# Kernel tuning notes

Measured on AMD Instinct MI355X. Metric: run time of the kernel, lower is better.

Reference implementation:

```python
import jax, jax.numpy as jnp
import numpy as np

B, H, S, D = 1, 16, 2048, 128
NUM_DOCS = 4


def setup_inputs() -> dict:
    key = jax.random.key(0)
    kq, kk, kv = jax.random.split(key, 3)
    q = jax.random.normal(kq, (B, H, S, D), dtype=jnp.float32)
    k = jax.random.normal(kk, (B, H, S, D), dtype=jnp.float32)
    v = jax.random.normal(kv, (B, H, S, D), dtype=jnp.float32)
    # Document boundaries within the packed sequence (as produced by _get_offsets):
    # starts at 0, ends at total token count. 4 equal docs of length 512.
    offsets = jnp.array([0, 512, 1024, 1536, 2048], dtype=jnp.int64)
    return {"q": q, "k": k, "v": v, "offsets": offsets}


def reference(q, k, v, offsets):
    # Block-causal SDPA: token i attends to token j iff j <= i and both are
    # in the same document (documents delimited by `offsets`). This matches
    # nested-tensor SDPA with is_causal=True over the jagged documents.
    _, _, S_, D_ = q.shape
    pos = jnp.arange(S_)
    seg = jnp.searchsorted(offsets, pos, side="right")  # [S] document id per token
    mask = (seg[:, None] == seg[None, :]) & (pos[None, :] <= pos[:, None])  # [S,S]
    scale = 1.0 / jnp.sqrt(jnp.asarray(D_, q.dtype))
    scores = jnp.einsum("bhsd,bhtd->bhst", q, k) * scale  # [B,H,S,S]
    scores = jnp.where(mask[None, None], scores, jnp.finfo(q.dtype).min)
    attn = jax.nn.softmax(scores, axis=-1)
    return jnp.einsum("bhst,bhtd->bhsd", attn, v)
```

## Files before the change

kernel.cpp:

```cpp
#include <hip/hip_runtime.h>
#include <hip/hip_bf16.h>
#include <math.h>

#define NH 16
#define SL 2048
#define DM 128
#define KVB 64

typedef float f32x4 __attribute__((ext_vector_type(4)));
typedef short s16x8 __attribute__((ext_vector_type(8)));
typedef short s16x4 __attribute__((ext_vector_type(4)));

static __device__ __forceinline__ short f2bf(float f) {
  __hip_bfloat16 h = __float2bfloat16(f);
  return __builtin_bit_cast(short, h);
}

__global__ __launch_bounds__(256) void attn_mfma(
    const float* __restrict__ qg,
    const float* __restrict__ kg,
    const float* __restrict__ vg,
    const int* __restrict__ offs, int n_off,
    float* __restrict__ out)
{
  __shared__ __align__(16) char Kb[64 * 128 * 2];
  __shared__ __align__(16) char Vb[128 * 64 * 2];
  __shared__ __align__(16) char Pb[4][16 * 64 * 2];

  const int t    = threadIdx.x;
  const int lane = t & 63;
  const int w    = t >> 6;
  const int col  = lane & 15;
  const int g    = lane >> 4;

  const int h  = blockIdx.x & 15;
  const int qb = 31 - (blockIdx.x >> 4);
  const int q0 = qb * 64;

  const float* qh = qg + (size_t)h * SL * DM;
  const float* kh = kg + (size_t)h * SL * DM;
  const float* vh = vg + (size_t)h * SL * DM;

  const float scale = 0.08838834764831843f;

  const int qrow = q0 + 16 * w + col;
  int qstart = 0;
  for (int i = 0; i < n_off; ++i) { int o = offs[i]; if (o <= qrow) qstart = o; }
  int kv_lo = 0;
  for (int i = 0; i < n_off; ++i) { int o = offs[i]; if (o <= q0) kv_lo = o; }

  s16x8 qf[4];
  #pragma unroll
  for (int kk = 0; kk < 4; ++kk) {
    const float* qp = qh + (size_t)qrow * DM + 32 * kk + 8 * g;
    f32x4 lo = *(const f32x4*)qp;
    f32x4 hi = *(const f32x4*)(qp + 4);
    s16x8 f;
    f[0] = f2bf(lo[0] * scale); f[1] = f2bf(lo[1] * scale);
    f[2] = f2bf(lo[2] * scale); f[3] = f2bf(lo[3] * scale);
    f[4] = f2bf(hi[0] * scale); f[5] = f2bf(hi[1] * scale);
    f[6] = f2bf(hi[2] * scale); f[7] = f2bf(hi[3] * scale);
    qf[kk] = f;
  }

  f32x4 acc[8];
  #pragma unroll
  for (int dt = 0; dt < 8; ++dt) { f32x4 z = {0.f, 0.f, 0.f, 0.f}; acc[dt] = z; }
  float m_ = -1e30f, l_ = 0.f;

  char* pb = &Pb[w][0];

  for (int kv0 = kv_lo; kv0 < q0 + 64; kv0 += KVB) {
    {
      const float* ks = kh + (size_t)kv0 * DM;
      const float* vs = vh + (size_t)kv0 * DM;
      const int d0 = (t & 31) * 4;
      const int r0 = t >> 5;
      #pragma unroll
      for (int ri = 0; ri < 8; ++ri) {
        int r = r0 + 8 * ri;
        f32x4 f = *(const f32x4*)(ks + (size_t)r * DM + d0);
        s16x4 b;
        b[0] = f2bf(f[0]); b[1] = f2bf(f[1]); b[2] = f2bf(f[2]); b[3] = f2bf(f[3]);
        *(s16x4*)(Kb + ((r * 256 + d0 * 2) ^ ((r & 7) << 4))) = b;
      }
      const int rot = (t >> 1) & 3;
      #pragma unroll
      for (int ki = 0; ki < 2; ++ki) {
        int k0 = r0 * 4 + 32 * ki;
        f32x4 a0 = *(const f32x4*)(vs + (size_t)(k0 + 0) * DM + d0);
        f32x4 a1 = *(const f32x4*)(vs + (size_t)(k0 + 1) * DM + d0);
        f32x4 a2 = *(const f32x4*)(vs + (size_t)(k0 + 2) * DM + d0);
        f32x4 a3 = *(const f32x4*)(vs + (size_t)(k0 + 3) * DM + d0);
        #pragma unroll
        for (int di = 0; di < 4; ++di) {
          int dd = (di + rot) & 3;
          int d = d0 + dd;
          s16x4 b;
          b[0] = f2bf(a0[dd]); b[1] = f2bf(a1[dd]); b[2] = f2bf(a2[dd]); b[3] = f2bf(a3[dd]);
          *(s16x4*)(Vb + ((d * 128 + k0 * 2) ^ ((d & 7) << 4))) = b;
        }
      }
    }
    __syncthreads();

    f32x4 st[4];
    #pragma unroll
    for (int kt = 0; kt < 4; ++kt) { f32x4 z = {0.f, 0.f, 0.f, 0.f}; st[kt] = z; }
    __builtin_amdgcn_s_setprio(1);
    #pragma unroll
    for (int kt = 0; kt < 4; ++kt) {
      int row = kt * 16 + col;
      #pragma unroll
      for (int kk = 0; kk < 4; ++kk) {
        s16x8 kf = *(const s16x8*)(Kb + ((row * 256 + 64 * kk + 16 * g) ^ ((row & 7) << 4)));
        st[kt] = __builtin_amdgcn_mfma_f32_16x16x32_bf16(kf, qf[kk], st[kt], 0, 0, 0);
      }
    }
    __builtin_amdgcn_s_setprio(0);

    float cm = -3.0e38f;
    #pragma unroll
    for (int kt = 0; kt < 4; ++kt) {
      #pragma unroll
      for (int r = 0; r < 4; ++r) {
        int kpos = kv0 + kt * 16 + 4 * g + r;
        float x = st[kt][r];
        bool ok = (kpos <= qrow) && (kpos >= qstart);
        x = ok ? x : -3.0e38f;
        st[kt][r] = x;
        cm = fmaxf(cm, x);
      }
    }
    cm = fmaxf(cm, __shfl_xor(cm, 16));
    cm = fmaxf(cm, __shfl_xor(cm, 32));
    float mn = fmaxf(m_, cm);
    float al = __expf(m_ - mn);
    m_ = mn;
    float psum = 0.f;
    #pragma unroll
    for (int kt = 0; kt < 4; ++kt) {
      s16x4 pk;
      #pragma unroll
      for (int r = 0; r < 4; ++r) {
        float p = __expf(st[kt][r] - mn);
        psum += p;
        pk[r] = f2bf(p);
      }
      *(s16x4*)(pb + ((col * 128 + 32 * kt + 8 * g) ^ ((col & 7) << 4))) = pk;
    }
    psum += __shfl_xor(psum, 16);
    psum += __shfl_xor(psum, 32);
    l_ = l_ * al + psum;

    #pragma unroll
    for (int r = 0; r < 4; ++r) {
      float ar = __shfl(al, 4 * g + r);
      #pragma unroll
      for (int dt = 0; dt < 8; ++dt) acc[dt][r] *= ar;
    }

    asm volatile("s_waitcnt lgkmcnt(0)" ::: "memory");
    __builtin_amdgcn_sched_barrier(0);

    __builtin_amdgcn_s_setprio(1);
    #pragma unroll
    for (int ksel = 0; ksel < 2; ++ksel) {
      s16x8 pa = *(const s16x8*)(pb + ((col * 128 + 64 * ksel + 16 * g) ^ ((col & 7) << 4)));
      #pragma unroll
      for (int dt = 0; dt < 8; ++dt) {
        int d = dt * 16 + col;
        s16x8 vf = *(const s16x8*)(Vb + ((d * 128 + 64 * ksel + 16 * g) ^ ((d & 7) << 4)));
        acc[dt] = __builtin_amdgcn_mfma_f32_16x16x32_bf16(pa, vf, acc[dt], 0, 0, 0);
      }
    }
    __builtin_amdgcn_s_setprio(0);
    __syncthreads();
  }

  #pragma unroll
  for (int r = 0; r < 4; ++r) {
    float lr  = __shfl(l_, 4 * g + r);
    float inv = 1.f / lr;
    int row   = q0 + 16 * w + 4 * g + r;
    float* op = out + ((size_t)h * SL + row) * DM + col;
    #pragma unroll
    for (int dt = 0; dt < 8; ++dt) op[dt * 16] = acc[dt][r] * inv;
  }
}

extern "C" void kernel_launch(void* const* d_in, const int* in_sizes, int n_in,
                              void* d_out, int out_size, void* d_ws, size_t ws_size,
                              hipStream_t stream) {
  const float* q = (const float*)d_in[0];
  const float* k = (const float*)d_in[1];
  const float* v = (const float*)d_in[2];
  const int* offs = (const int*)d_in[3];
  const int n_off = in_sizes[3];
  float* out = (float*)d_out;

  const int blocks = NH * (SL / 64);
  attn_mfma<<<blocks, 256, 0, stream>>>(q, k, v, offs, n_off, out);
}
```

Baseline: 31.34 us.

## Pre-convert K/V to swizzled bf16 and double-buffer tiles via global_load_lds

Adds a separate pre-pass kernel that converts K and V to bf16 once, into the pre-swizzled shared-memory layout in workspace. The attention kernel then streams these tiles straight into double-buffered LDS with global_load_lds, prefetching the next tile while it computes the current one. This removes the repeated per-block fp32 load and convert work and overlaps loads with compute. The price is an extra kernel launch, an extra round trip of K/V through global memory, and doubled LDS use that may lower occupancy. It also remaps the block index so work is interleaved within each document, and keeps a fallback kernel for when the workspace is too small.

```diff
diff --git a/kernel.cpp b/kernel.cpp
--- a/kernel.cpp
+++ b/kernel.cpp
@@ -5,7 +5,6 @@
 #define NH 16
 #define SL 2048
 #define DM 128
-#define KVB 64
 
 typedef float f32x4 __attribute__((ext_vector_type(4)));
 typedef short s16x8 __attribute__((ext_vector_type(8)));
@@ -16,7 +15,227 @@
   return __builtin_bit_cast(short, h);
 }
 
-__global__ __launch_bounds__(256) void attn_mfma(
+__global__ __launch_bounds__(256) void convert_kv(
+    const float* __restrict__ kg, const float* __restrict__ vg,
+    char* __restrict__ kbf, char* __restrict__ vbf)
+{
+  const int t = threadIdx.x;
+  const int h = blockIdx.x & 15;
+  const int T = blockIdx.x >> 4;
+  const float* ks = kg + ((size_t)h * SL + (size_t)T * 64) * DM;
+  const float* vs = vg + ((size_t)h * SL + (size_t)T * 64) * DM;
+  char* kc = kbf + (((size_t)h * 32 + T) << 14);
+  char* vc = vbf + (((size_t)h * 32 + T) << 14);
+  const int d0 = (t & 31) * 4;
+  const int r0 = t >> 5;
+  #pragma unroll
+  for (int ri = 0; ri < 8; ++ri) {
+    int r = r0 + 8 * ri;
+    f32x4 f = *(const f32x4*)(ks + (size_t)r * DM + d0);
+    s16x4 b;
+    b[0] = f2bf(f[0]); b[1] = f2bf(f[1]); b[2] = f2bf(f[2]); b[3] = f2bf(f[3]);
+    *(s16x4*)(kc + ((r * 256 + d0 * 2) ^ ((r & 7) << 4))) = b;
+  }
+  #pragma unroll
+  for (int ki = 0; ki < 2; ++ki) {
+    int k0 = r0 * 4 + 32 * ki;
+    f32x4 a0 = *(const f32x4*)(vs + (size_t)(k0 + 0) * DM + d0);
+    f32x4 a1 = *(const f32x4*)(vs + (size_t)(k0 + 1) * DM + d0);
+    f32x4 a2 = *(const f32x4*)(vs + (size_t)(k0 + 2) * DM + d0);
+    f32x4 a3 = *(const f32x4*)(vs + (size_t)(k0 + 3) * DM + d0);
+    #pragma unroll
+    for (int dd = 0; dd < 4; ++dd) {
+      int d = d0 + dd;
+      s16x4 b;
+      b[0] = f2bf(a0[dd]); b[1] = f2bf(a1[dd]); b[2] = f2bf(a2[dd]); b[3] = f2bf(a3[dd]);
+      *(s16x4*)(vc + ((d * 128 + k0 * 2) ^ ((d & 7) << 4))) = b;
+    }
+  }
+}
+
+#define GLDS16(gsrc, lbase) \
+  __builtin_amdgcn_global_load_lds( \
+      (const __attribute__((address_space(1))) void*)(gsrc), \
+      (__attribute__((address_space(3))) void*)(lbase), 16, 0, 0)
+
+__global__ __launch_bounds__(256) void attn_mfma2(
+    const float* __restrict__ qg,
+    const char* __restrict__ kbf, const char* __restrict__ vbf,
+    const int* __restrict__ offs, int n_off,
+    float* __restrict__ out)
+{
+  __shared__ __align__(16) char Kb[2][16384];
+  __shared__ __align__(16) char Vb[2][16384];
+  __shared__ __align__(16) char Pb[4][2048];
+
+  const int t    = threadIdx.x;
+  const int lane = t & 63;
+  const int w    = t >> 6;
+  const int col  = lane & 15;
+  const int g    = lane >> 4;
+
+  const int blk = blockIdx.x;
+  const int z = blk >> 8;
+  const int y = (blk >> 4) & 15;
+  const int h = blk & 15;
+  const int dno = y >> 2, u = y & 3;
+  const int p = z ? u : 7 - u;
+  const int q0 = (dno * 8 + p) * 64;
+
+  const float* qh = qg + (size_t)h * SL * DM;
+  const float scale = 0.08838834764831843f;
+
+  const int qrow = q0 + 16 * w + col;
+  int qstart = 0;
+  for (int i = 0; i < n_off; ++i) { int o = offs[i]; if (o <= qrow) qstart = o; }
+  int kv_lo = 0;
+  for (int i = 0; i < n_off; ++i) { int o = offs[i]; if (o <= q0) kv_lo = o; }
+  const int ntiles = ((q0 + 64) - kv_lo) >> 6;
+  const int T0 = kv_lo >> 6;
+
+  const char* kc = kbf + (((size_t)h * 32) << 14);
+  const char* vc = vbf + (((size_t)h * 32) << 14);
+
+#define STAGE(T, B) do {                                                     \
+    const char* _ks = kc + (((size_t)(T)) << 14);                            \
+    const char* _vs = vc + (((size_t)(T)) << 14);                            \
+    _Pragma("unroll")                                                        \
+    for (int _i = 0; _i < 4; ++_i) {                                         \
+      const int _lo = (w + 4 * _i) << 10;                                    \
+      GLDS16(_ks + _lo + lane * 16, &Kb[B][_lo]);                            \
+      GLDS16(_vs + _lo + lane * 16, &Vb[B][_lo]);                            \
+    }                                                                        \
+  } while (0)
+
+  f32x4 qlo[4], qhi[4];
+  #pragma unroll
+  for (int kk = 0; kk < 4; ++kk) {
+    const float* qp = qh + (size_t)qrow * DM + 32 * kk + 8 * g;
+    qlo[kk] = *(const f32x4*)qp;
+    qhi[kk] = *(const f32x4*)(qp + 4);
+  }
+
+  STAGE(T0, 0);
+
+  s16x8 qf[4];
+  #pragma unroll
+  for (int kk = 0; kk < 4; ++kk) {
+    s16x8 f;
+    f[0] = f2bf(qlo[kk][0] * scale); f[1] = f2bf(qlo[kk][1] * scale);
+    f[2] = f2bf(qlo[kk][2] * scale); f[3] = f2bf(qlo[kk][3] * scale);
+    f[4] = f2bf(qhi[kk][0] * scale); f[5] = f2bf(qhi[kk][1] * scale);
+    f[6] = f2bf(qhi[kk][2] * scale); f[7] = f2bf(qhi[kk][3] * scale);
+    qf[kk] = f;
+  }
+
+  f32x4 acc[8];
+  #pragma unroll
+  for (int dt = 0; dt < 8; ++dt) { f32x4 zv = {0.f, 0.f, 0.f, 0.f}; acc[dt] = zv; }
+  float m_ = -1e30f, l_ = 0.f;
+
+  char* pb = &Pb[w][0];
+  int buf = 0;
+
+  for (int it = 0; it < ntiles; ++it) {
+    const int kv0 = kv_lo + (it << 6);
+    if (it + 1 < ntiles) {
+      STAGE(T0 + it + 1, buf ^ 1);
+      asm volatile("s_waitcnt vmcnt(8)" ::: "memory");
+    } else {
+      asm volatile("s_waitcnt vmcnt(0)" ::: "memory");
+    }
+    __builtin_amdgcn_sched_barrier(0);
+    __builtin_amdgcn_s_barrier();
+
+    f32x4 st[4];
+    #pragma unroll
+    for (int kt = 0; kt < 4; ++kt) { f32x4 zv = {0.f, 0.f, 0.f, 0.f}; st[kt] = zv; }
+    __builtin_amdgcn_s_setprio(1);
+    #pragma unroll
+    for (int kt = 0; kt < 4; ++kt) {
+      int row = kt * 16 + col;
+      #pragma unroll
+      for (int kk = 0; kk < 4; ++kk) {
+        s16x8 kf = *(const s16x8*)(&Kb[buf][0] + ((row * 256 + 64 * kk + 16 * g) ^ ((row & 7) << 4)));
+        st[kt] = __builtin_amdgcn_mfma_f32_16x16x32_bf16(kf, qf[kk], st[kt], 0, 0, 0);
+      }
+    }
+    __builtin_amdgcn_s_setprio(0);
+
+    float cm = -3.0e38f;
+    #pragma unroll
+    for (int kt = 0; kt < 4; ++kt) {
+      #pragma unroll
+      for (int r = 0; r < 4; ++r) {
+        int kpos = kv0 + kt * 16 + 4 * g + r;
+        float x = st[kt][r];
+        bool ok = (kpos <= qrow) && (kpos >= qstart);
+        x = ok ? x : -3.0e38f;
+        st[kt][r] = x;
+        cm = fmaxf(cm, x);
+      }
+    }
+    cm = fmaxf(cm, __shfl_xor(cm, 16));
+    cm = fmaxf(cm, __shfl_xor(cm, 32));
+    float mn = fmaxf(m_, cm);
+    float al = __expf(m_ - mn);
+    m_ = mn;
+    float psum = 0.f;
+    #pragma unroll
+    for (int kt = 0; kt < 4; ++kt) {
+      s16x4 pk;
+      #pragma unroll
+      for (int r = 0; r < 4; ++r) {
+        float pe = __expf(st[kt][r] - mn);
+        psum += pe;
+        pk[r] = f2bf(pe);
+      }
+      *(s16x4*)(pb + ((col * 128 + 32 * kt + 8 * g) ^ ((col & 7) << 4))) = pk;
+    }
+    psum += __shfl_xor(psum, 16);
+    psum += __shfl_xor(psum, 32);
+    l_ = l_ * al + psum;
+
+    #pragma unroll
+    for (int r = 0; r < 4; ++r) {
+      float ar = __shfl(al, 4 * g + r);
+      #pragma unroll
+      for (int dt = 0; dt < 8; ++dt) acc[dt][r] *= ar;
+    }
+
+    asm volatile("s_waitcnt lgkmcnt(0)" ::: "memory");
+    __builtin_amdgcn_sched_barrier(0);
+
+    __builtin_amdgcn_s_setprio(1);
+    #pragma unroll
+    for (int ksel = 0; ksel < 2; ++ksel) {
+      s16x8 pa = *(const s16x8*)(pb + ((col * 128 + 64 * ksel + 16 * g) ^ ((col & 7) << 4)));
+      #pragma unroll
+      for (int dt = 0; dt < 8; ++dt) {
+        int d = dt * 16 + col;
+        s16x8 vf = *(const s16x8*)(&Vb[buf][0] + ((d * 128 + 64 * ksel + 16 * g) ^ ((d & 7) << 4)));
+        acc[dt] = __builtin_amdgcn_mfma_f32_16x16x32_bf16(pa, vf, acc[dt], 0, 0, 0);
+      }
+    }
+    __builtin_amdgcn_s_setprio(0);
+    __builtin_amdgcn_sched_barrier(0);
+    __builtin_amdgcn_s_barrier();
+    buf ^= 1;
+  }
+#undef STAGE
+
+  #pragma unroll
+  for (int r = 0; r < 4; ++r) {
+    float lr  = __shfl(l_, 4 * g + r);
+    float inv = 1.f / lr;
+    int row   = q0 + 16 * w + 4 * g + r;
+    float* op = out + ((size_t)h * SL + row) * DM + col;
+    #pragma unroll
+    for (int dt = 0; dt < 8; ++dt) op[dt * 16] = acc[dt][r] * inv;
+  }
+}
+
+__global__ __launch_bounds__(256) void attn_mfma_fb(
     const float* __restrict__ qg,
     const float* __restrict__ kg,
     const float* __restrict__ vg,
@@ -65,12 +284,11 @@
 
   f32x4 acc[8];
   #pragma unroll
-  for (int dt = 0; dt < 8; ++dt) { f32x4 z = {0.f, 0.f, 0.f, 0.f}; acc[dt] = z; }
+  for (int dt = 0; dt < 8; ++dt) { f32x4 zv = {0.f, 0.f, 0.f, 0.f}; acc[dt] = zv; }
   float m_ = -1e30f, l_ = 0.f;
-
   char* pb = &Pb[w][0];
 
-  for (int kv0 = kv_lo; kv0 < q0 + 64; kv0 += KVB) {
+  for (int kv0 = kv_lo; kv0 < q0 + 64; kv0 += 64) {
     {
       const float* ks = kh + (size_t)kv0 * DM;
       const float* vs = vh + (size_t)kv0 * DM;
@@ -106,8 +324,7 @@
 
     f32x4 st[4];
     #pragma unroll
-    for (int kt = 0; kt < 4; ++kt) { f32x4 z = {0.f, 0.f, 0.f, 0.f}; st[kt] = z; }
-    __builtin_amdgcn_s_setprio(1);
+    for (int kt = 0; kt < 4; ++kt) { f32x4 zv = {0.f, 0.f, 0.f, 0.f}; st[kt] = zv; }
     #pragma unroll
     for (int kt = 0; kt < 4; ++kt) {
       int row = kt * 16 + col;
@@ -117,7 +334,6 @@
         st[kt] = __builtin_amdgcn_mfma_f32_16x16x32_bf16(kf, qf[kk], st[kt], 0, 0, 0);
       }
     }
-    __builtin_amdgcn_s_setprio(0);
 
     float cm = -3.0e38f;
     #pragma unroll
@@ -143,9 +359,9 @@
       s16x4 pk;
       #pragma unroll
       for (int r = 0; r < 4; ++r) {
-        float p = __expf(st[kt][r] - mn);
-        psum += p;
-        pk[r] = f2bf(p);
+        float pe = __expf(st[kt][r] - mn);
+        psum += pe;
+        pk[r] = f2bf(pe);
       }
       *(s16x4*)(pb + ((col * 128 + 32 * kt + 8 * g) ^ ((col & 7) << 4))) = pk;
     }
@@ -163,7 +379,6 @@
     asm volatile("s_waitcnt lgkmcnt(0)" ::: "memory");
     __builtin_amdgcn_sched_barrier(0);
 
-    __builtin_amdgcn_s_setprio(1);
     #pragma unroll
     for (int ksel = 0; ksel < 2; ++ksel) {
       s16x8 pa = *(const s16x8*)(pb + ((col * 128 + 64 * ksel + 16 * g) ^ ((col & 7) << 4)));
@@ -174,7 +389,6 @@
         acc[dt] = __builtin_amdgcn_mfma_f32_16x16x32_bf16(pa, vf, acc[dt], 0, 0, 0);
       }
     }
-    __builtin_amdgcn_s_setprio(0);
     __syncthreads();
   }
 
@@ -199,6 +413,13 @@
   const int n_off = in_sizes[3];
   float* out = (float*)d_out;
 
-  const int blocks = NH * (SL / 64);
-  attn_mfma<<<blocks, 256, 0, stream>>>(q, k, v, offs, n_off, out);
+  const size_t chunk_bytes = (size_t)NH * 32 * 16384;
+  if (ws_size >= 2 * chunk_bytes) {
+    char* kbf = (char*)d_ws;
+    char* vbf = kbf + chunk_bytes;
+    convert_kv<<<NH * 32, 256, 0, stream>>>(k, v, kbf, vbf);
+    attn_mfma2<<<512, 256, 0, stream>>>(q, kbf, vbf, offs, n_off, out);
+  } else {
+    attn_mfma_fb<<<512, 256, 0, stream>>>(q, k, v, offs, n_off, out);
+  }
 }
```

Measured after the change: 35.78 us. +14.2%, slower.

## Split KV range across two warp-groups per block and merge softmax partials

Applied to the files above, without the earlier changes.

Doubles the block to 512 threads. Two halves of four waves each process disjoint halves of the KV tiles for the same 64 query rows, each with its own K/V shared-memory buffers. At the end the two partial accumulators and their (m, l) statistics are merged through shared memory using a log-sum-exp combine. This shortens the serial KV loop per block, aimed at the long-tail blocks near document ends, at the cost of a larger block, more shared memory, idle waves when the tile count is odd, and an extra merge step.

```diff
diff --git a/kernel.cpp b/kernel.cpp
--- a/kernel.cpp
+++ b/kernel.cpp
@@ -5,7 +5,6 @@
 #define NH 16
 #define SL 2048
 #define DM 128
-#define KVB 64
 
 typedef float f32x4 __attribute__((ext_vector_type(4)));
 typedef short s16x8 __attribute__((ext_vector_type(8)));
@@ -16,26 +15,28 @@
   return __builtin_bit_cast(short, h);
 }
 
-__global__ __launch_bounds__(256) void attn_mfma(
+__global__ __launch_bounds__(512) void attn_split(
     const float* __restrict__ qg,
     const float* __restrict__ kg,
     const float* __restrict__ vg,
     const int* __restrict__ offs, int n_off,
     float* __restrict__ out)
 {
-  __shared__ __align__(16) char Kb[64 * 128 * 2];
-  __shared__ __align__(16) char Vb[128 * 64 * 2];
-  __shared__ __align__(16) char Pb[4][16 * 64 * 2];
+  __shared__ __align__(16) char Kb[2][16384];
+  __shared__ __align__(16) char Vb[2][16384];
+  __shared__ __align__(16) char Pb[8][2048];
 
   const int t    = threadIdx.x;
   const int lane = t & 63;
   const int w    = t >> 6;
   const int col  = lane & 15;
   const int g    = lane >> 4;
+  const int half = w >> 2;
+  const int wq   = w & 3;
+  const int th   = t & 255;
 
   const int h  = blockIdx.x & 15;
-  const int qb = 31 - (blockIdx.x >> 4);
-  const int q0 = qb * 64;
+  const int q0 = (31 - (blockIdx.x >> 4)) * 64;
 
   const float* qh = qg + (size_t)h * SL * DM;
   const float* kh = kg + (size_t)h * SL * DM;
@@ -43,11 +44,13 @@
 
   const float scale = 0.08838834764831843f;
 
-  const int qrow = q0 + 16 * w + col;
+  const int qrow = q0 + 16 * wq + col;
   int qstart = 0;
   for (int i = 0; i < n_off; ++i) { int o = offs[i]; if (o <= qrow) qstart = o; }
   int kv_lo = 0;
   for (int i = 0; i < n_off; ++i) { int o = offs[i]; if (o <= q0) kv_lo = o; }
+  const int n  = ((q0 + 64) - kv_lo) >> 6;
+  const int nh = (n + 1) >> 1;
 
   s16x8 qf[4];
   #pragma unroll
@@ -65,26 +68,32 @@
 
   f32x4 acc[8];
   #pragma unroll
-  for (int dt = 0; dt < 8; ++dt) { f32x4 z = {0.f, 0.f, 0.f, 0.f}; acc[dt] = z; }
+  for (int dt = 0; dt < 8; ++dt) { f32x4 zv = {0.f, 0.f, 0.f, 0.f}; acc[dt] = zv; }
   float m_ = -1e30f, l_ = 0.f;
 
   char* pb = &Pb[w][0];
-
-  for (int kv0 = kv_lo; kv0 < q0 + 64; kv0 += KVB) {
-    {
+  char* kb = &Kb[half][0];
+  char* vb = &Vb[half][0];
+
+  for (int it = 0; it < nh; ++it) {
+    const int T   = half ? (nh + it) : it;
+    const bool act = (T < n);
+    const int kv0 = kv_lo + (T << 6);
+
+    if (act) {
       const float* ks = kh + (size_t)kv0 * DM;
       const float* vs = vh + (size_t)kv0 * DM;
-      const int d0 = (t & 31) * 4;
-      const int r0 = t >> 5;
+      const int d0 = (th & 31) * 4;
+      const int r0 = th >> 5;
       #pragma unroll
       for (int ri = 0; ri < 8; ++ri) {
         int r = r0 + 8 * ri;
         f32x4 f = *(const f32x4*)(ks + (size_t)r * DM + d0);
         s16x4 b;
         b[0] = f2bf(f[0]); b[1] = f2bf(f[1]); b[2] = f2bf(f[2]); b[3] = f2bf(f[3]);
-        *(s16x4*)(Kb + ((r * 256 + d0 * 2) ^ ((r & 7) << 4))) = b;
-      }
-      const int rot = (t >> 1) & 3;
+        *(s16x4*)(kb + ((r * 256 + d0 * 2) ^ ((r & 7) << 4))) = b;
+      }
+      const int rot = (th >> 1) & 3;
       #pragma unroll
       for (int ki = 0; ki < 2; ++ki) {
         int k0 = r0 * 4 + 32 * ki;
@@ -98,94 +107,115 @@
           int d = d0 + dd;
           s16x4 b;
           b[0] = f2bf(a0[dd]); b[1] = f2bf(a1[dd]); b[2] = f2bf(a2[dd]); b[3] = f2bf(a3[dd]);
-          *(s16x4*)(Vb + ((d * 128 + k0 * 2) ^ ((d & 7) << 4))) = b;
+          *(s16x4*)(vb + ((d * 128 + k0 * 2) ^ ((d & 7) << 4))) = b;
         }
       }
     }
     __syncthreads();
 
-    f32x4 st[4];
+    if (act) {
+      f32x4 st[4];
+      #pragma unroll
+      for (int kt = 0; kt < 4; ++kt) { f32x4 zv = {0.f, 0.f, 0.f, 0.f}; st[kt] = zv; }
+      __builtin_amdgcn_s_setprio(1);
+      #pragma unroll
+      for (int kt = 0; kt < 4; ++kt) {
+        int row = kt * 16 + col;
+        #pragma unroll
+        for (int kk = 0; kk < 4; ++kk) {
+          s16x8 kf = *(const s16x8*)(kb + ((row * 256 + 64 * kk + 16 * g) ^ ((row & 7) << 4)));
+          st[kt] = __builtin_amdgcn_mfma_f32_16x16x32_bf16(kf, qf[kk], st[kt], 0, 0, 0);
+        }
+      }
+      __builtin_amdgcn_s_setprio(0);
+
+      float cm = -3.0e38f;
+      #pragma unroll
+      for (int kt = 0; kt < 4; ++kt) {
+        #pragma unroll
+        for (int r = 0; r < 4; ++r) {
+          int kpos = kv0 + kt * 16 + 4 * g + r;
+          float x = st[kt][r];
+          bool ok = (kpos <= qrow) && (kpos >= qstart);
+          x = ok ? x : -3.0e38f;
+          st[kt][r] = x;
+          cm = fmaxf(cm, x);
+        }
+      }
+      cm = fmaxf(cm, __shfl_xor(cm, 16));
+      cm = fmaxf(cm, __shfl_xor(cm, 32));
+      float mn = fmaxf(m_, cm);
+      float al = __expf(m_ - mn);
+      m_ = mn;
+      float psum = 0.f;
+      #pragma unroll
+      for (int kt = 0; kt < 4; ++kt) {
+        s16x4 pk;
+        #pragma unroll
+        for (int r = 0; r < 4; ++r) {
+          float pe = __expf(st[kt][r] - mn);
+          psum += pe;
+          pk[r] = f2bf(pe);
+        }
+        *(s16x4*)(pb + ((col * 128 + 32 * kt + 8 * g) ^ ((col & 7) << 4))) = pk;
+      }
+      psum += __shfl_xor(psum, 16);
+      psum += __shfl_xor(psum, 32);
+      l_ = l_ * al + psum;
+
+      #pragma unroll
+      for (int r = 0; r < 4; ++r) {
+        float ar = __shfl(al, 4 * g + r);
+        #pragma unroll
+        for (int dt = 0; dt < 8; ++dt) acc[dt][r] *= ar;
+      }
+
+      asm volatile("s_waitcnt lgkmcnt(0)" ::: "memory");
+      __builtin_amdgcn_sched_barrier(0);
+
+      __builtin_amdgcn_s_setprio(1);
+      #pragma unroll
+      for (int ksel = 0; ksel < 2; ++ksel) {
+        s16x8 pa = *(const s16x8*)(pb + ((col * 128 + 64 * ksel + 16 * g) ^ ((col & 7) << 4)));
+        #pragma unroll
+        for (int dt = 0; dt < 8; ++dt) {
+          int d = dt * 16 + col;
+          s16x8 vf = *(const s16x8*)(vb + ((d * 128 + 64 * ksel + 16 * g) ^ ((d & 7) << 4)));
+          acc[dt] = __builtin_amdgcn_mfma_f32_16x16x32_bf16(pa, vf, acc[dt], 0, 0, 0);
+        }
+      }
+      __builtin_amdgcn_s_setprio(0);
+    }
+    __syncthreads();
+  }
+
+  char* mac = &Kb[0][0];
+  char* mml = &Vb[0][0];
+  if (half) {
     #pragma unroll
-    for (int kt = 0; kt < 4; ++kt) { f32x4 z = {0.f, 0.f, 0.f, 0.f}; st[kt] = z; }
-    __builtin_amdgcn_s_setprio(1);
+    for (int dt = 0; dt < 8; ++dt)
+      *(f32x4*)(mac + (wq * 64 + lane) * 128 + ((dt ^ (lane & 7)) * 16)) = acc[dt];
+    *(float2*)(mml + (wq * 64 + lane) * 8) = make_float2(m_, l_);
+  }
+  __syncthreads();
+  if (!half) {
+    float2 ml = *(const float2*)(mml + (wq * 64 + lane) * 8);
+    float mm   = fmaxf(m_, ml.x);
+    float eA   = __expf(m_ - mm);
+    float eB   = __expf(ml.x - mm);
+    float linv = 1.f / (l_ * eA + ml.y * eB);
+    float fa = eA * linv, fb = eB * linv;
     #pragma unroll
-    for (int kt = 0; kt < 4; ++kt) {
-      int row = kt * 16 + col;
-      #pragma unroll
-      for (int kk = 0; kk < 4; ++kk) {
-        s16x8 kf = *(const s16x8*)(Kb + ((row * 256 + 64 * kk + 16 * g) ^ ((row & 7) << 4)));
-        st[kt] = __builtin_amdgcn_mfma_f32_16x16x32_bf16(kf, qf[kk], st[kt], 0, 0, 0);
+    for (int dt = 0; dt < 8; ++dt) {
+      f32x4 aB = *(const f32x4*)(mac + (wq * 64 + lane) * 128 + ((dt ^ (lane & 7)) * 16));
+      #pragma unroll
+      for (int r = 0; r < 4; ++r) {
+        float a = __shfl(fa, 4 * g + r);
+        float b = __shfl(fb, 4 * g + r);
+        int row = q0 + 16 * wq + 4 * g + r;
+        out[((size_t)h * SL + row) * DM + dt * 16 + col] = acc[dt][r] * a + aB[r] * b;
       }
     }
-    __builtin_amdgcn_s_setprio(0);
-
-    float cm = -3.0e38f;
-    #pragma unroll
-    for (int kt = 0; kt < 4; ++kt) {
-      #pragma unroll
-      for (int r = 0; r < 4; ++r) {
-        int kpos = kv0 + kt * 16 + 4 * g + r;
-        float x = st[kt][r];
-        bool ok = (kpos <= qrow) && (kpos >= qstart);
-        x = ok ? x : -3.0e38f;
-        st[kt][r] = x;
-        cm = fmaxf(cm, x);
-      }
-    }
-    cm = fmaxf(cm, __shfl_xor(cm, 16));
-    cm = fmaxf(cm, __shfl_xor(cm, 32));
-    float mn = fmaxf(m_, cm);
-    float al = __expf(m_ - mn);
-    m_ = mn;
-    float psum = 0.f;
-    #pragma unroll
-    for (int kt = 0; kt < 4; ++kt) {
-      s16x4 pk;
-      #pragma unroll
-      for (int r = 0; r < 4; ++r) {
-        float p = __expf(st[kt][r] - mn);
-        psum += p;
-        pk[r] = f2bf(p);
-      }
-      *(s16x4*)(pb + ((col * 128 + 32 * kt + 8 * g) ^ ((col & 7) << 4))) = pk;
-    }
-    psum += __shfl_xor(psum, 16);
-    psum += __shfl_xor(psum, 32);
-    l_ = l_ * al + psum;
-
-    #pragma unroll
-    for (int r = 0; r < 4; ++r) {
-      float ar = __shfl(al, 4 * g + r);
-      #pragma unroll
-      for (int dt = 0; dt < 8; ++dt) acc[dt][r] *= ar;
-    }
-
-    asm volatile("s_waitcnt lgkmcnt(0)" ::: "memory");
-    __builtin_amdgcn_sched_barrier(0);
-
-    __builtin_amdgcn_s_setprio(1);
-    #pragma unroll
-    for (int ksel = 0; ksel < 2; ++ksel) {
-      s16x8 pa = *(const s16x8*)(pb + ((col * 128 + 64 * ksel + 16 * g) ^ ((col & 7) << 4)));
-      #pragma unroll
-      for (int dt = 0; dt < 8; ++dt) {
-        int d = dt * 16 + col;
-        s16x8 vf = *(const s16x8*)(Vb + ((d * 128 + 64 * ksel + 16 * g) ^ ((d & 7) << 4)));
-        acc[dt] = __builtin_amdgcn_mfma_f32_16x16x32_bf16(pa, vf, acc[dt], 0, 0, 0);
-      }
-    }
-    __builtin_amdgcn_s_setprio(0);
-    __syncthreads();
-  }
-
-  #pragma unroll
-  for (int r = 0; r < 4; ++r) {
-    float lr  = __shfl(l_, 4 * g + r);
-    float inv = 1.f / lr;
-    int row   = q0 + 16 * w + 4 * g + r;
-    float* op = out + ((size_t)h * SL + row) * DM + col;
-    #pragma unroll
-    for (int dt = 0; dt < 8; ++dt) op[dt * 16] = acc[dt][r] * inv;
   }
 }
 
@@ -200,5 +230,5 @@
   float* out = (float*)d_out;
 
   const int blocks = NH * (SL / 64);
-  attn_mfma<<<blocks, 256, 0, stream>>>(q, k, v, offs, n_off, out);
+  attn_split<<<blocks, 512, 0, stream>>>(q, k, v, offs, n_off, out);
 }
```

After: 45.21 us. 44.3% more time.

## Double-buffer K/V tiles with register prefetch and reorder query blocks

Applied to the files above, without the earlier changes.

Splits the K/V tile staging into a global-to-register load issued at the start of each iteration and a register-to-LDS bf16 write at the end, into alternating LDS buffers. This lets global load latency overlap the QK and PV MFMA work and removes one barrier per iteration. It also remaps block indices so the heavier query blocks of each 512-token document are launched first, for better load balance. The cost is doubled K/V LDS use, which lowers how many blocks fit per CU, plus extra registers held across the loop.

```diff
diff --git a/kernel.cpp b/kernel.cpp
--- a/kernel.cpp
+++ b/kernel.cpp
@@ -5,7 +5,6 @@
 #define NH 16
 #define SL 2048
 #define DM 128
-#define KVB 64
 
 typedef float f32x4 __attribute__((ext_vector_type(4)));
 typedef short s16x8 __attribute__((ext_vector_type(8)));
@@ -16,16 +15,16 @@
   return __builtin_bit_cast(short, h);
 }
 
-__global__ __launch_bounds__(256) void attn_mfma(
+__global__ __launch_bounds__(256) void attn_dbuf(
     const float* __restrict__ qg,
     const float* __restrict__ kg,
     const float* __restrict__ vg,
     const int* __restrict__ offs, int n_off,
     float* __restrict__ out)
 {
-  __shared__ __align__(16) char Kb[64 * 128 * 2];
-  __shared__ __align__(16) char Vb[128 * 64 * 2];
-  __shared__ __align__(16) char Pb[4][16 * 64 * 2];
+  __shared__ __align__(16) char Kb[2][16384];
+  __shared__ __align__(16) char Vb[2][16384];
+  __shared__ __align__(16) char Pb[4][2048];
 
   const int t    = threadIdx.x;
   const int lane = t & 63;
@@ -33,9 +32,13 @@
   const int col  = lane & 15;
   const int g    = lane >> 4;
 
-  const int h  = blockIdx.x & 15;
-  const int qb = 31 - (blockIdx.x >> 4);
-  const int q0 = qb * 64;
+  const int blk = blockIdx.x;
+  const int z   = blk >> 8;
+  const int y   = (blk >> 4) & 15;
+  const int h   = blk & 15;
+  const int dno = y >> 2, u = y & 3;
+  const int p   = z ? u : 7 - u;
+  const int q0  = (dno * 8 + p) * 64;
 
   const float* qh = qg + (size_t)h * SL * DM;
   const float* kh = kg + (size_t)h * SL * DM;
@@ -48,6 +51,7 @@
   for (int i = 0; i < n_off; ++i) { int o = offs[i]; if (o <= qrow) qstart = o; }
   int kv_lo = 0;
   for (int i = 0; i < n_off; ++i) { int o = offs[i]; if (o <= q0) kv_lo = o; }
+  const int n = ((q0 + 64) - kv_lo) >> 6;
 
   s16x8 qf[4];
   #pragma unroll
@@ -65,55 +69,77 @@
 
   f32x4 acc[8];
   #pragma unroll
-  for (int dt = 0; dt < 8; ++dt) { f32x4 z = {0.f, 0.f, 0.f, 0.f}; acc[dt] = z; }
+  for (int dt = 0; dt < 8; ++dt) { f32x4 zv = {0.f, 0.f, 0.f, 0.f}; acc[dt] = zv; }
   float m_ = -1e30f, l_ = 0.f;
 
   char* pb = &Pb[w][0];
 
-  for (int kv0 = kv_lo; kv0 < q0 + 64; kv0 += KVB) {
-    {
-      const float* ks = kh + (size_t)kv0 * DM;
-      const float* vs = vh + (size_t)kv0 * DM;
-      const int d0 = (t & 31) * 4;
-      const int r0 = t >> 5;
-      #pragma unroll
-      for (int ri = 0; ri < 8; ++ri) {
-        int r = r0 + 8 * ri;
-        f32x4 f = *(const f32x4*)(ks + (size_t)r * DM + d0);
-        s16x4 b;
-        b[0] = f2bf(f[0]); b[1] = f2bf(f[1]); b[2] = f2bf(f[2]); b[3] = f2bf(f[3]);
-        *(s16x4*)(Kb + ((r * 256 + d0 * 2) ^ ((r & 7) << 4))) = b;
-      }
-      const int rot = (t >> 1) & 3;
-      #pragma unroll
-      for (int ki = 0; ki < 2; ++ki) {
-        int k0 = r0 * 4 + 32 * ki;
-        f32x4 a0 = *(const f32x4*)(vs + (size_t)(k0 + 0) * DM + d0);
-        f32x4 a1 = *(const f32x4*)(vs + (size_t)(k0 + 1) * DM + d0);
-        f32x4 a2 = *(const f32x4*)(vs + (size_t)(k0 + 2) * DM + d0);
-        f32x4 a3 = *(const f32x4*)(vs + (size_t)(k0 + 3) * DM + d0);
-        #pragma unroll
-        for (int di = 0; di < 4; ++di) {
-          int dd = (di + rot) & 3;
-          int d = d0 + dd;
-          s16x4 b;
-          b[0] = f2bf(a0[dd]); b[1] = f2bf(a1[dd]); b[2] = f2bf(a2[dd]); b[3] = f2bf(a3[dd]);
-          *(s16x4*)(Vb + ((d * 128 + k0 * 2) ^ ((d & 7) << 4))) = b;
-        }
-      }
-    }
+  const int d0  = (t & 31) * 4;
+  const int r0  = t >> 5;
+  const int rot = (t >> 1) & 3;
+  f32x4 kr[8], vr[8];
+
+#define LOADT(T) do {                                                         \
+    const float* _ks = kh + (size_t)(kv_lo + ((T) << 6)) * DM;                \
+    const float* _vs = vh + (size_t)(kv_lo + ((T) << 6)) * DM;                \
+    _Pragma("unroll")                                                         \
+    for (int _i = 0; _i < 8; ++_i)                                            \
+      kr[_i] = *(const f32x4*)(_ks + (size_t)(r0 + 8 * _i) * DM + d0);        \
+    _Pragma("unroll")                                                         \
+    for (int _k = 0; _k < 2; ++_k) {                                          \
+      _Pragma("unroll")                                                       \
+      for (int _j = 0; _j < 4; ++_j)                                          \
+        vr[_k * 4 + _j] =                                                     \
+          *(const f32x4*)(_vs + (size_t)(r0 * 4 + 32 * _k + _j) * DM + d0);   \
+    }                                                                         \
+  } while (0)
+
+#define WRITEKV(B) do {                                                       \
+    _Pragma("unroll")                                                         \
+    for (int _i = 0; _i < 8; ++_i) {                                          \
+      int _r = r0 + 8 * _i;                                                   \
+      s16x4 _b;                                                               \
+      _b[0] = f2bf(kr[_i][0]); _b[1] = f2bf(kr[_i][1]);                       \
+      _b[2] = f2bf(kr[_i][2]); _b[3] = f2bf(kr[_i][3]);                       \
+      *(s16x4*)(&Kb[B][0] + ((_r * 256 + d0 * 2) ^ ((_r & 7) << 4))) = _b;    \
+    }                                                                         \
+    _Pragma("unroll")                                                         \
+    for (int _k = 0; _k < 2; ++_k) {                                          \
+      int _k0 = r0 * 4 + 32 * _k;                                             \
+      _Pragma("unroll")                                                       \
+      for (int _di = 0; _di < 4; ++_di) {                                     \
+        int _dd = (_di + rot) & 3;                                            \
+        int _d  = d0 + _dd;                                                   \
+        s16x4 _b;                                                             \
+        _b[0] = f2bf(vr[_k * 4 + 0][_dd]); _b[1] = f2bf(vr[_k * 4 + 1][_dd]); \
+        _b[2] = f2bf(vr[_k * 4 + 2][_dd]); _b[3] = f2bf(vr[_k * 4 + 3][_dd]); \
+        *(s16x4*)(&Vb[B][0] + ((_d * 128 + _k0 * 2) ^ ((_d & 7) << 4))) = _b; \
+      }                                                                       \
+    }                                                                         \
+  } while (0)
+
+  LOADT(0);
+  WRITEKV(0);
+  int cur = 0;
+
+  for (int it = 0; it < n; ++it) {
+    const int kv0 = kv_lo + (it << 6);
     __syncthreads();
 
+    const bool pre = (it + 1 < n);
+    if (pre) LOADT(it + 1);
+    __builtin_amdgcn_sched_barrier(0);
+
     f32x4 st[4];
     #pragma unroll
-    for (int kt = 0; kt < 4; ++kt) { f32x4 z = {0.f, 0.f, 0.f, 0.f}; st[kt] = z; }
+    for (int kt = 0; kt < 4; ++kt) { f32x4 zv = {0.f, 0.f, 0.f, 0.f}; st[kt] = zv; }
     __builtin_amdgcn_s_setprio(1);
     #pragma unroll
     for (int kt = 0; kt < 4; ++kt) {
       int row = kt * 16 + col;
       #pragma unroll
       for (int kk = 0; kk < 4; ++kk) {
-        s16x8 kf = *(const s16x8*)(Kb + ((row * 256 + 64 * kk + 16 * g) ^ ((row & 7) << 4)));
+        s16x8 kf = *(const s16x8*)(&Kb[cur][0] + ((row * 256 + 64 * kk + 16 * g) ^ ((row & 7) << 4)));
         st[kt] = __builtin_amdgcn_mfma_f32_16x16x32_bf16(kf, qf[kk], st[kt], 0, 0, 0);
       }
     }
@@ -143,9 +169,9 @@
       s16x4 pk;
       #pragma unroll
       for (int r = 0; r < 4; ++r) {
-        float p = __expf(st[kt][r] - mn);
-        psum += p;
-        pk[r] = f2bf(p);
+        float pe = __expf(st[kt][r] - mn);
+        psum += pe;
+        pk[r] = f2bf(pe);
       }
       *(s16x4*)(pb + ((col * 128 + 32 * kt + 8 * g) ^ ((col & 7) << 4))) = pk;
     }
@@ -170,13 +196,17 @@
       #pragma unroll
       for (int dt = 0; dt < 8; ++dt) {
         int d = dt * 16 + col;
-        s16x8 vf = *(const s16x8*)(Vb + ((d * 128 + 64 * ksel + 16 * g) ^ ((d & 7) << 4)));
+        s16x8 vf = *(const s16x8*)(&Vb[cur][0] + ((d * 128 + 64 * ksel + 16 * g) ^ ((d & 7) << 4)));
         acc[dt] = __builtin_amdgcn_mfma_f32_16x16x32_bf16(pa, vf, acc[dt], 0, 0, 0);
       }
     }
     __builtin_amdgcn_s_setprio(0);
-    __syncthreads();
+
+    if (pre) WRITEKV(cur ^ 1);
+    cur ^= 1;
   }
+#undef LOADT
+#undef WRITEKV
 
   #pragma unroll
   for (int r = 0; r < 4; ++r) {
@@ -200,5 +230,5 @@
   float* out = (float*)d_out;
 
   const int blocks = NH * (SL / 64);
-  attn_mfma<<<blocks, 256, 0, stream>>>(q, k, v, offs, n_off, out);
+  attn_dbuf<<<blocks, 256, 0, stream>>>(q, k, v, offs, n_off, out);
 }
```

New measurement: 29.28 us. -6.6%, faster.
